# Kernel optimization log

Measured on AMD Instinct MI355X. Metric: run time of the kernel, lower is better.

Reference implementation:

```python
import jax, jax.numpy as jnp
import numpy as np

OBS_LEN = 8
PRED_LEN = 12
BATCH = 65536
EMB = 64
H = 64


def setup_inputs() -> dict:
    key = jax.random.key(0)
    ks = jax.random.split(key, 18)
    s = 1.0 / np.sqrt(H)  # torch default uniform bound scale, used as std here

    def p(k, shape):
        return (jax.random.normal(k, shape, dtype=jnp.float32) * s).astype(jnp.float32)

    return {
        "obs_traj": jax.random.normal(ks[0], (OBS_LEN, BATCH, 2), dtype=jnp.float32),
        "obs_traj_rel": jax.random.normal(ks[1], (OBS_LEN, BATCH, 2), dtype=jnp.float32),
        # encoder params
        "enc_emb_w": p(ks[2], (EMB, 2)),
        "enc_emb_b": p(ks[3], (EMB,)),
        "enc_w_ih": p(ks[4], (4 * H, EMB)),
        "enc_w_hh": p(ks[5], (4 * H, H)),
        "enc_b_ih": p(ks[6], (4 * H,)),
        "enc_b_hh": p(ks[7], (4 * H,)),
        # decoder params
        "dec_emb_w": p(ks[8], (EMB, 2)),
        "dec_emb_b": p(ks[9], (EMB,)),
        "dec_w_ih": p(ks[10], (4 * H, EMB)),
        "dec_w_hh": p(ks[11], (4 * H, H)),
        "dec_b_ih": p(ks[12], (4 * H,)),
        "dec_b_hh": p(ks[13], (4 * H,)),
        "h2p_w": p(ks[14], (2, H)),
        "h2p_b": p(ks[15], (2,)),
    }


def _lstm_cell(h, c, x, w_ih, w_hh, b_ih, b_hh):
    # torch nn.LSTM gate order: i, f, g, o
    gates = x @ w_ih.T + h @ w_hh.T + (b_ih + b_hh)
    i, f, g, o = jnp.split(gates, 4, axis=-1)
    c_new = jax.nn.sigmoid(f) * c + jax.nn.sigmoid(i) * jnp.tanh(g)
    h_new = jax.nn.sigmoid(o) * jnp.tanh(c_new)
    return h_new, c_new


def reference(obs_traj, obs_traj_rel,
              enc_emb_w, enc_emb_b, enc_w_ih, enc_w_hh, enc_b_ih, enc_b_hh,
              dec_emb_w, dec_emb_b, dec_w_ih, dec_w_hh, dec_b_ih, dec_b_hh,
              h2p_w, h2p_b):
    batch = obs_traj_rel.shape[1]

    # ---------- Encoder ----------
    enc_in = obs_traj_rel @ enc_emb_w.T + enc_emb_b  # [T, B, EMB]

    def enc_step(carry, x_t):
        h, c = carry
        h, c = _lstm_cell(h, c, x_t, enc_w_ih, enc_w_hh, enc_b_ih, enc_b_hh)
        return (h, c), None

    h0 = jnp.zeros((batch, H), dtype=obs_traj_rel.dtype)
    c0 = jnp.zeros((batch, H), dtype=obs_traj_rel.dtype)
    (h_enc, _), _ = jax.lax.scan(enc_step, (h0, c0), enc_in)

    # ---------- Decoder ----------
    dec_h = h_enc                                   # final encoder hidden seeds decoder
    dec_c = jnp.zeros((batch, H), dtype=obs_traj_rel.dtype)
    last_pos_rel = obs_traj_rel[-1]
    dec_in = last_pos_rel @ dec_emb_w.T + dec_emb_b  # [B, EMB]

    def dec_step(carry, _):
        h, c, x = carry
        h, c = _lstm_cell(h, c, x, dec_w_ih, dec_w_hh, dec_b_ih, dec_b_hh)
        rel_pos = h @ h2p_w.T + h2p_b               # [B, 2]
        x_next = rel_pos @ dec_emb_w.T + dec_emb_b  # [B, EMB]
        return (h, c, x_next), rel_pos

    (_, _, _), pred_traj_fake_rel = jax.lax.scan(
        dec_step, (dec_h, dec_c, dec_in), None, length=PRED_LEN)
    return pred_traj_fake_rel  # [PRED_LEN, B, 2]
```

## Files before the change

### kernel.cpp

```cpp
#include <hip/hip_runtime.h>

#define OBS_LEN 8
#define PRED_LEN 12
#define TILE_B 128
#define NTHREADS 512

typedef __attribute__((ext_vector_type(8))) short short8;
typedef __attribute__((ext_vector_type(4))) float floatx4;
typedef __attribute__((ext_vector_type(2))) float floatx2;
typedef __attribute__((ext_vector_type(4))) unsigned int u32x4;
typedef __attribute__((ext_vector_type(2))) unsigned int u32x2;
typedef unsigned short u16;
typedef unsigned int u32;

#define L2E 1.442695040888963f

__device__ __forceinline__ u16 f2bf(float f) {
  __bf16 b = (__bf16)f;
  return __builtin_bit_cast(u16, b);
}

#if __has_builtin(__builtin_amdgcn_exp2f)
__device__ __forceinline__ float fexp2_(float x) { return __builtin_amdgcn_exp2f(x); }
#else
__device__ __forceinline__ float fexp2_(float x) { return exp2f(x); }
#endif
__device__ __forceinline__ floatx2 exp2v(floatx2 x) {
  floatx2 r;
  r.x = fexp2_(x.x);
  r.y = fexp2_(x.y);
  return r;
}
#if __has_builtin(__builtin_amdgcn_rcpf)
__device__ __forceinline__ floatx2 rcp2(floatx2 x) {
  floatx2 r;
  r.x = __builtin_amdgcn_rcpf(x.x);
  r.y = __builtin_amdgcn_rcpf(x.y);
  return r;
}
#else
__device__ __forceinline__ floatx2 rcp2(floatx2 x) {
  return floatx2{1.0f / x.x, 1.0f / x.y};
}
#endif

__device__ __forceinline__ floatx4 mfma_bf(short8 a, short8 b, floatx4 c) {
  return __builtin_amdgcn_mfma_f32_16x16x32_bf16(a, b, c, 0, 0, 0);
}

__device__ __forceinline__ short8 frag_lo(u32 a) {
  return __builtin_bit_cast(short8, u32x4{a, 0u, 0u, 0u});
}

__device__ __forceinline__ void fold_rank2(const float* __restrict__ wr,
                                           const float* __restrict__ emb_w,
                                           const float* __restrict__ emb_b,
                                           float& A0, float& A1, float& B0) {
  A0 = A1 = B0 = 0.f;
#pragma unroll
  for (int e4 = 0; e4 < 16; ++e4) {
    const floatx4 w = *(const floatx4*)(wr + e4 * 4);
    const floatx4 m0 = *(const floatx4*)(emb_w + e4 * 8);
    const floatx4 m1 = *(const floatx4*)(emb_w + e4 * 8 + 4);
    const floatx4 bb = *(const floatx4*)(emb_b + e4 * 4);
    A0 += w[0] * m0[0] + w[1] * m0[2] + w[2] * m1[0] + w[3] * m1[2];
    A1 += w[0] * m0[1] + w[1] * m0[3] + w[2] * m1[1] + w[3] * m1[3];
    B0 += w[0] * bb[0] + w[1] * bb[1] + w[2] * bb[2] + w[3] * bb[3];
  }
}

__device__ __forceinline__ void stage_w(const float* __restrict__ W,
                                        u16* __restrict__ wS, int tid) {
  for (int slot = tid; slot < 2048; slot += NTHREADS) {
    const int lane = slot & 63, kf = (slot >> 6) & 1, tile = slot >> 7;
    const int g = lane >> 4, l16 = lane & 15;
    const int gate = (tile >> 2) * 64 + (tile & 3) * 16 + l16;
    const float* src = W + gate * 64 + kf * 32 + g * 8;
    const floatx4 w0 = *(const floatx4*)src;
    const floatx4 w1 = *(const floatx4*)(src + 4);
    short8 a;
#pragma unroll
    for (int j = 0; j < 4; ++j) {
      a[j] = (short)f2bf(w0[j]);
      a[j + 4] = (short)f2bf(w1[j]);
    }
    *(short8*)(wS + slot * 8) = a;
  }
}

__device__ __forceinline__ void stage_weff(const float* __restrict__ Whh,
                                           const float* __restrict__ dA0S,
                                           const float* __restrict__ dA1S,
                                           const float* __restrict__ hw0,
                                           const float* __restrict__ hw1,
                                           u16* __restrict__ wS, int tid) {
  for (int slot = tid; slot < 2048; slot += NTHREADS) {
    const int lane = slot & 63, kf = (slot >> 6) & 1, tile = slot >> 7;
    const int g = lane >> 4, l16 = lane & 15;
    const int gate = (tile >> 2) * 64 + (tile & 3) * 16 + l16;
    const int k0 = kf * 32 + g * 8;
    const float a0 = dA0S[gate], a1 = dA1S[gate];
    const float* src = Whh + gate * 64 + k0;
    const floatx4 w0 = *(const floatx4*)src;
    const floatx4 w1 = *(const floatx4*)(src + 4);
    const floatx4 p00 = *(const floatx4*)(hw0 + k0);
    const floatx4 p01 = *(const floatx4*)(hw0 + k0 + 4);
    const floatx4 p10 = *(const floatx4*)(hw1 + k0);
    const floatx4 p11 = *(const floatx4*)(hw1 + k0 + 4);
    short8 a;
#pragma unroll
    for (int j = 0; j < 4; ++j) {
      a[j] = (short)f2bf(w0[j] + a0 * p00[j] + a1 * p10[j]);
      a[j + 4] = (short)f2bf(w1[j] + a0 * p01[j] + a1 * p11[j]);
    }
    *(short8*)(wS + slot * 8) = a;
  }
}

__device__ __forceinline__ void nonlin_store_ut(const floatx4 (&acc)[4],
                                                floatx4& cc,
                                                u16* __restrict__ wrh,
                                                int l16, int g, int ut) {
  const int sw = l16 & 7;
  u32 hpk[2];
#pragma unroll
  for (int p = 0; p < 2; ++p) {
    const floatx2 iv = {acc[0][2 * p], acc[0][2 * p + 1]};
    const floatx2 fv = {acc[1][2 * p], acc[1][2 * p + 1]};
    const floatx2 gv = {acc[2][2 * p], acc[2][2 * p + 1]};
    const floatx2 ov = {acc[3][2 * p], acc[3][2 * p + 1]};
    const floatx2 ei = exp2v(iv * -L2E);
    const floatx2 ef = exp2v(fv * -L2E);
    const floatx2 eg = exp2v(gv * (2.0f * L2E));
    const floatx2 eo = exp2v(ov * -L2E);
    const floatx2 A = ei + 1.0f;
    const floatx2 F = ef + 1.0f;
    const floatx2 Bg = eg + 1.0f;
    const floatx2 P = A * Bg;
    const floatx2 cold = {cc[2 * p], cc[2 * p + 1]};
    const floatx2 num = cold * P + (eg - 1.0f) * F;
    const floatx2 cn = num * rcp2(F * P);
    cc[2 * p] = cn.x;
    cc[2 * p + 1] = cn.y;
    const floatx2 ec = exp2v(cn * (2.0f * L2E));
    const floatx2 h = (ec - 1.0f) * rcp2((eo + 1.0f) * (ec + 1.0f));
    hpk[p] = (u32)f2bf(h.x) | ((u32)f2bf(h.y) << 16);
  }
  *(u32x2*)(wrh + l16 * 64 + (((ut * 2 + (g >> 1)) ^ sw) * 8) + (g & 1) * 4) =
      u32x2{hpk[0], hpk[1]};
}

template <int PH>
__device__ __forceinline__ void ut_group(int ut, floatx4& cc,
                                         short8 hb0, short8 hb1, short8 pfv,
                                         const u16* __restrict__ wp,
                                         const u32* __restrict__ pafp,
                                         const float* __restrict__ biasp,
                                         u16* __restrict__ wrh,
                                         int g, int l16) {
  floatx4 acc[4];
#pragma unroll
  for (int tg = 0; tg < 4; ++tg) {
    const int tile = tg * 4 + ut;
    const floatx4 biasv = *(const floatx4*)(biasp + tg * 64 + ut * 16 + g * 4);
    if (PH == 0) {
      const u32 pa = (g == 0) ? pafp[tile * 16 + l16] : 0u;
      acc[tg] = mfma_bf(frag_lo(pa), pfv, biasv);
    } else {
      acc[tg] = biasv;
    }
    acc[tg] = mfma_bf(*(const short8*)(wp + (tile * 2 + 1) * 512), hb1, acc[tg]);
    acc[tg] = mfma_bf(*(const short8*)(wp + (tile * 2 + 0) * 512), hb0, acc[tg]);
  }
  nonlin_store_ut(acc, cc, wrh, l16, g, ut);
}

__global__ void __launch_bounds__(NTHREADS, 4)
lstm_kernel(const float* __restrict__ obs_rel,
            const float* __restrict__ enc_emb_w, const float* __restrict__ enc_emb_b,
            const float* __restrict__ enc_w_ih, const float* __restrict__ enc_w_hh,
            const float* __restrict__ enc_b_ih, const float* __restrict__ enc_b_hh,
            const float* __restrict__ dec_emb_w, const float* __restrict__ dec_emb_b,
            const float* __restrict__ dec_w_ih, const float* __restrict__ dec_w_hh,
            const float* __restrict__ dec_b_ih, const float* __restrict__ dec_b_hh,
            const float* __restrict__ h2p_w, const float* __restrict__ h2p_b,
            float* __restrict__ out, int batch) {
  __shared__ __align__(16) u16 wS[16384];
  __shared__ __align__(16) u16 hP[8 * 1024];
  __shared__ __align__(16) float biasS[3][256];
  __shared__ __align__(16) u32 pafS[2][256];
  __shared__ __align__(16) u32 posP[OBS_LEN * TILE_B];
  __shared__ __align__(16) float hw0S[64], hw1S[64];
  __shared__ __align__(16) float dA0S[256], dA1S[256];

  const int tid = threadIdx.x;
  const int wv = tid >> 6, lane = tid & 63;
  const int g = lane >> 4, l16 = lane & 15;
  const long S0 = (long)blockIdx.x * TILE_B;

  for (int i = tid; i < OBS_LEN * TILE_B; i += NTHREADS) {
    const int t = i >> 7, s = i & 127;
    const floatx2 pp = *(const floatx2*)(obs_rel + (long)t * batch * 2 + (S0 + s) * 2);
    posP[i] = (u32)f2bf(pp.x) | ((u32)f2bf(pp.y) << 16);
  }
  if (tid < 64) {
    hw0S[tid] = h2p_w[tid];
    hw1S[tid] = h2p_w[64 + tid];
  }
  const float hb2p0 = h2p_b[0], hb2p1 = h2p_b[1];
  if (tid < 256) {
    const int t = tid >> 6, u6 = tid & 63;
    const int pidx = (t * 4 + (u6 >> 4)) * 16 + (u6 & 15);
    float A0, A1, B0;
    fold_rank2(enc_w_ih + tid * 64, enc_emb_w, enc_emb_b, A0, A1, B0);
    pafS[0][pidx] = (u32)f2bf(A0) | ((u32)f2bf(A1) << 16);
    biasS[0][tid] = enc_b_ih[tid] + enc_b_hh[tid] + B0;
    fold_rank2(dec_w_ih + tid * 64, dec_emb_w, dec_emb_b, A0, A1, B0);
    pafS[1][pidx] = (u32)f2bf(A0) | ((u32)f2bf(A1) << 16);
    dA0S[tid] = A0;
    dA1S[tid] = A1;
    const float db = dec_b_ih[tid] + dec_b_hh[tid] + B0;
    biasS[1][tid] = db;
    biasS[2][tid] = db + A0 * hb2p0 + A1 * hb2p1;
  }
  stage_w(enc_w_hh, wS, tid);
  for (int i = tid; i < 4096; i += NTHREADS) ((u32*)hP)[i] = 0;
  __syncthreads();

  u16* hw = hP + wv * 1024;
  const u16* wp = wS + lane * 8;
  const int sw8 = l16 & 7;
  floatx4 c0{0.f, 0.f, 0.f, 0.f}, c1{0.f, 0.f, 0.f, 0.f};
  floatx4 c2v{0.f, 0.f, 0.f, 0.f}, c3{0.f, 0.f, 0.f, 0.f};

#pragma unroll 1
  for (int t = 0; t < OBS_LEN; ++t) {
    const u16* hr = hw + l16 * 64;
    const short8 hb0 = *(const short8*)(hr + ((g ^ sw8) * 8));
    const short8 hb1 = *(const short8*)(hr + (((4 + g) ^ sw8) * 8));
    const u32 pp = (g == 0) ? posP[t * TILE_B + wv * 16 + l16] : 0u;
    const short8 pfv = frag_lo(pp);
    ut_group<0>(0, c0, hb0, hb1, pfv, wp, &pafS[0][0], &biasS[0][0], hw, g, l16);
    __builtin_amdgcn_sched_barrier(0);
    ut_group<0>(1, c1, hb0, hb1, pfv, wp, &pafS[0][0], &biasS[0][0], hw, g, l16);
    __builtin_amdgcn_sched_barrier(0);
    ut_group<0>(2, c2v, hb0, hb1, pfv, wp, &pafS[0][0], &biasS[0][0], hw, g, l16);
    __builtin_amdgcn_sched_barrier(0);
    ut_group<0>(3, c3, hb0, hb1, pfv, wp, &pafS[0][0], &biasS[0][0], hw, g, l16);
  }

  __syncthreads();
  stage_w(dec_w_hh, wS, tid);
  __syncthreads();
  c0 = c1 = c2v = c3 = floatx4{0.f, 0.f, 0.f, 0.f};
  {
    const u16* hr = hw + l16 * 64;
    const short8 hb0 = *(const short8*)(hr + ((g ^ sw8) * 8));
    const short8 hb1 = *(const short8*)(hr + (((4 + g) ^ sw8) * 8));
    const u32 pp = (g == 0) ? posP[7 * TILE_B + wv * 16 + l16] : 0u;
    const short8 pfv = frag_lo(pp);
    ut_group<0>(0, c0, hb0, hb1, pfv, wp, &pafS[1][0], &biasS[1][0], hw, g, l16);
    __builtin_amdgcn_sched_barrier(0);
    ut_group<0>(1, c1, hb0, hb1, pfv, wp, &pafS[1][0], &biasS[1][0], hw, g, l16);
    __builtin_amdgcn_sched_barrier(0);
    ut_group<0>(2, c2v, hb0, hb1, pfv, wp, &pafS[1][0], &biasS[1][0], hw, g, l16);
    __builtin_amdgcn_sched_barrier(0);
    ut_group<0>(3, c3, hb0, hb1, pfv, wp, &pafS[1][0], &biasS[1][0], hw, g, l16);
  }
  __syncthreads();
  stage_weff(dec_w_hh, dA0S, dA1S, hw0S, hw1S, wS, tid);
  __syncthreads();

  short8 xf0, xf1;
#pragma unroll
  for (int kf = 0; kf < 2; ++kf) {
    const int kb = kf * 32 + g * 8;
    short8 a;
#pragma unroll
    for (int j = 0; j < 8; ++j) {
      const float r = (l16 == 0) ? hw0S[kb + j] : (l16 == 1) ? hw1S[kb + j] : 0.f;
      a[j] = (short)f2bf(r);
    }
    if (kf == 0) xf0 = a; else xf1 = a;
  }

  const floatx4 zero4{0.f, 0.f, 0.f, 0.f};
#pragma unroll 1
  for (int j = 1; j < PRED_LEN; ++j) {
    const u16* hr = hw + l16 * 64;
    const short8 hb0 = *(const short8*)(hr + ((g ^ sw8) * 8));
    const short8 hb1 = *(const short8*)(hr + (((4 + g) ^ sw8) * 8));
    floatx4 ar = mfma_bf(xf0, hb0, zero4);
    ar = mfma_bf(xf1, hb1, ar);
    if (g == 0)
      *(floatx2*)(out + (long)(j - 1) * batch * 2 + (S0 + wv * 16 + l16) * 2) =
          floatx2{ar[0] + hb2p0, ar[1] + hb2p1};
    ut_group<1>(0, c0, hb0, hb1, xf0, wp, &pafS[1][0], &biasS[2][0], hw, g, l16);
    __builtin_amdgcn_sched_barrier(0);
    ut_group<1>(1, c1, hb0, hb1, xf0, wp, &pafS[1][0], &biasS[2][0], hw, g, l16);
    __builtin_amdgcn_sched_barrier(0);
    ut_group<1>(2, c2v, hb0, hb1, xf0, wp, &pafS[1][0], &biasS[2][0], hw, g, l16);
    __builtin_amdgcn_sched_barrier(0);
    ut_group<1>(3, c3, hb0, hb1, xf0, wp, &pafS[1][0], &biasS[2][0], hw, g, l16);
  }

  {
    const u16* hr = hw + l16 * 64;
    const short8 hb0 = *(const short8*)(hr + ((g ^ sw8) * 8));
    const short8 hb1 = *(const short8*)(hr + (((4 + g) ^ sw8) * 8));
    floatx4 ar = mfma_bf(xf0, hb0, zero4);
    ar = mfma_bf(xf1, hb1, ar);
    if (g == 0)
      *(floatx2*)(out + (long)(PRED_LEN - 1) * batch * 2 + (S0 + wv * 16 + l16) * 2) =
          floatx2{ar[0] + hb2p0, ar[1] + hb2p1};
  }
}

extern "C" void kernel_launch(void* const* d_in, const int* in_sizes, int n_in,
                              void* d_out, int out_size, void* d_ws, size_t ws_size,
                              hipStream_t stream) {
  const float* obs_rel = (const float*)d_in[1];
  const int batch = in_sizes[1] / (OBS_LEN * 2);

  const int blocks = batch / TILE_B;
  hipLaunchKernelGGL(lstm_kernel, dim3(blocks), dim3(NTHREADS), 0, stream,
                     obs_rel,
                     (const float*)d_in[2], (const float*)d_in[3],
                     (const float*)d_in[4], (const float*)d_in[5],
                     (const float*)d_in[6], (const float*)d_in[7],
                     (const float*)d_in[8], (const float*)d_in[9],
                     (const float*)d_in[10], (const float*)d_in[11],
                     (const float*)d_in[12], (const float*)d_in[13],
                     (const float*)d_in[14], (const float*)d_in[15],
                     (float*)d_out, batch);
}
```

Measured before the change: 196.4 us.

## Keep recurrent weights in registers and give each wave two batch subtiles

Blocks shrink to 256 threads (4 waves), and each wave now handles 32 batch rows as two 16-row chunks instead of one. The W_hh MFMA fragments are loaded once per phase into a 32-entry short8 register array. They are reused across both chunks and all timesteps, which removes the per-step LDS weight reads. The cost is much higher VGPR pressure, with launch bounds relaxed to 2 blocks per CU, so fewer resident waves remain to hide MFMA, transcendental and LDS latency.

```diff
diff --git a/kernel.cpp b/kernel.cpp
--- a/kernel.cpp
+++ b/kernel.cpp
@@ -3,7 +3,7 @@
 #define OBS_LEN 8
 #define PRED_LEN 12
 #define TILE_B 128
-#define NTHREADS 512
+#define NTHREADS 256
 
 typedef __attribute__((ext_vector_type(8))) short short8;
 typedef __attribute__((ext_vector_type(4))) float floatx4;
@@ -117,11 +117,19 @@
   }
 }
 
+__device__ __forceinline__ void load_wf(const u16* __restrict__ wp,
+                                        short8 (&wf)[16][2]) {
+#pragma unroll
+  for (int tile = 0; tile < 16; ++tile)
+#pragma unroll
+    for (int kf = 0; kf < 2; ++kf)
+      wf[tile][kf] = *(const short8*)(wp + (tile * 2 + kf) * 512);
+}
+
 __device__ __forceinline__ void nonlin_store_ut(const floatx4 (&acc)[4],
                                                 floatx4& cc,
-                                                u16* __restrict__ wrh,
-                                                int l16, int g, int ut) {
-  const int sw = l16 & 7;
+                                                u16* __restrict__ wrow,
+                                                int g, int ut, int sw) {
   u32 hpk[2];
 #pragma unroll
   for (int p = 0; p < 2; ++p) {
@@ -146,36 +154,58 @@
     const floatx2 h = (ec - 1.0f) * rcp2((eo + 1.0f) * (ec + 1.0f));
     hpk[p] = (u32)f2bf(h.x) | ((u32)f2bf(h.y) << 16);
   }
-  *(u32x2*)(wrh + l16 * 64 + (((ut * 2 + (g >> 1)) ^ sw) * 8) + (g & 1) * 4) =
+  *(u32x2*)(wrow + (((ut * 2 + (g >> 1)) ^ sw) * 8) + (g & 1) * 4) =
       u32x2{hpk[0], hpk[1]};
 }
 
-template <int PH>
-__device__ __forceinline__ void ut_group(int ut, floatx4& cc,
-                                         short8 hb0, short8 hb1, short8 pfv,
-                                         const u16* __restrict__ wp,
-                                         const u32* __restrict__ pafp,
-                                         const float* __restrict__ biasp,
-                                         u16* __restrict__ wrh,
-                                         int g, int l16) {
-  floatx4 acc[4];
-#pragma unroll
-  for (int tg = 0; tg < 4; ++tg) {
-    const int tile = tg * 4 + ut;
-    const floatx4 biasv = *(const floatx4*)(biasp + tg * 64 + ut * 16 + g * 4);
+template <int PH, int REL>
+__device__ __forceinline__ void step_all(
+    const short8 (&wf)[16][2], floatx4 (&c)[8], u16* __restrict__ hw,
+    const u32* __restrict__ pafp, const float* __restrict__ biasp,
+    const u32* __restrict__ posrow, short8 xf0, short8 xf1,
+    float hb2p0, float hb2p1, float* __restrict__ outp, long sbase,
+    int wv, int g, int l16, int sw8) {
+#pragma unroll
+  for (int n = 0; n < 2; ++n) {
+    u16* wrow = hw + (n * 16 + l16) * 64;
+    const short8 hb0 = *(const short8*)(wrow + ((g ^ sw8) * 8));
+    const short8 hb1 = *(const short8*)(wrow + (((4 + g) ^ sw8) * 8));
+    short8 pfv = short8{0, 0, 0, 0, 0, 0, 0, 0};
     if (PH == 0) {
-      const u32 pa = (g == 0) ? pafp[tile * 16 + l16] : 0u;
-      acc[tg] = mfma_bf(frag_lo(pa), pfv, biasv);
-    } else {
-      acc[tg] = biasv;
-    }
-    acc[tg] = mfma_bf(*(const short8*)(wp + (tile * 2 + 1) * 512), hb1, acc[tg]);
-    acc[tg] = mfma_bf(*(const short8*)(wp + (tile * 2 + 0) * 512), hb0, acc[tg]);
-  }
-  nonlin_store_ut(acc, cc, wrh, l16, g, ut);
-}
-
-__global__ void __launch_bounds__(NTHREADS, 4)
+      const u32 pp = (g == 0) ? posrow[wv * 32 + n * 16 + l16] : 0u;
+      pfv = frag_lo(pp);
+    }
+    if (REL) {
+      floatx4 ar = mfma_bf(xf0, hb0, floatx4{0.f, 0.f, 0.f, 0.f});
+      ar = mfma_bf(xf1, hb1, ar);
+      if (g == 0)
+        *(floatx2*)(outp + (sbase + n * 16 + l16) * 2) =
+            floatx2{ar[0] + hb2p0, ar[1] + hb2p1};
+    }
+#pragma unroll
+    for (int ut = 0; ut < 4; ++ut) {
+      floatx4 acc[4];
+#pragma unroll
+      for (int tg = 0; tg < 4; ++tg) {
+        const int tile = tg * 4 + ut;
+        const floatx4 biasv =
+            *(const floatx4*)(biasp + tg * 64 + ut * 16 + g * 4);
+        if (PH == 0) {
+          const u32 pa = (g == 0) ? pafp[tile * 16 + l16] : 0u;
+          acc[tg] = mfma_bf(frag_lo(pa), pfv, biasv);
+        } else {
+          acc[tg] = biasv;
+        }
+        acc[tg] = mfma_bf(wf[tile][1], hb1, acc[tg]);
+        acc[tg] = mfma_bf(wf[tile][0], hb0, acc[tg]);
+      }
+      nonlin_store_ut(acc, c[n * 4 + ut], wrow, g, ut, sw8);
+      __builtin_amdgcn_sched_barrier(0);
+    }
+  }
+}
+
+__global__ void __launch_bounds__(NTHREADS, 2)
 lstm_kernel(const float* __restrict__ obs_rel,
             const float* __restrict__ enc_emb_w, const float* __restrict__ enc_emb_b,
             const float* __restrict__ enc_w_ih, const float* __restrict__ enc_w_hh,
@@ -186,7 +216,7 @@
             const float* __restrict__ h2p_w, const float* __restrict__ h2p_b,
             float* __restrict__ out, int batch) {
   __shared__ __align__(16) u16 wS[16384];
-  __shared__ __align__(16) u16 hP[8 * 1024];
+  __shared__ __align__(16) u16 hP[4 * 2048];
   __shared__ __align__(16) float biasS[3][256];
   __shared__ __align__(16) u32 pafS[2][256];
   __shared__ __align__(16) u32 posP[OBS_LEN * TILE_B];
@@ -208,7 +238,7 @@
     hw1S[tid] = h2p_w[64 + tid];
   }
   const float hb2p0 = h2p_b[0], hb2p1 = h2p_b[1];
-  if (tid < 256) {
+  {
     const int t = tid >> 6, u6 = tid & 63;
     const int pidx = (t * 4 + (u6 >> 4)) * 16 + (u6 & 15);
     float A0, A1, B0;
@@ -227,49 +257,36 @@
   for (int i = tid; i < 4096; i += NTHREADS) ((u32*)hP)[i] = 0;
   __syncthreads();
 
-  u16* hw = hP + wv * 1024;
+  u16* hw = hP + wv * 2048;
   const u16* wp = wS + lane * 8;
   const int sw8 = l16 & 7;
-  floatx4 c0{0.f, 0.f, 0.f, 0.f}, c1{0.f, 0.f, 0.f, 0.f};
-  floatx4 c2v{0.f, 0.f, 0.f, 0.f}, c3{0.f, 0.f, 0.f, 0.f};
+  const long sbase = S0 + wv * 32;
+
+  short8 wf[16][2];
+  load_wf(wp, wf);
+  floatx4 c[8];
+#pragma unroll
+  for (int i = 0; i < 8; ++i) c[i] = floatx4{0.f, 0.f, 0.f, 0.f};
+  const short8 z8 = short8{0, 0, 0, 0, 0, 0, 0, 0};
 
 #pragma unroll 1
   for (int t = 0; t < OBS_LEN; ++t) {
-    const u16* hr = hw + l16 * 64;
-    const short8 hb0 = *(const short8*)(hr + ((g ^ sw8) * 8));
-    const short8 hb1 = *(const short8*)(hr + (((4 + g) ^ sw8) * 8));
-    const u32 pp = (g == 0) ? posP[t * TILE_B + wv * 16 + l16] : 0u;
-    const short8 pfv = frag_lo(pp);
-    ut_group<0>(0, c0, hb0, hb1, pfv, wp, &pafS[0][0], &biasS[0][0], hw, g, l16);
-    __builtin_amdgcn_sched_barrier(0);
-    ut_group<0>(1, c1, hb0, hb1, pfv, wp, &pafS[0][0], &biasS[0][0], hw, g, l16);
-    __builtin_amdgcn_sched_barrier(0);
-    ut_group<0>(2, c2v, hb0, hb1, pfv, wp, &pafS[0][0], &biasS[0][0], hw, g, l16);
-    __builtin_amdgcn_sched_barrier(0);
-    ut_group<0>(3, c3, hb0, hb1, pfv, wp, &pafS[0][0], &biasS[0][0], hw, g, l16);
+    step_all<0, 0>(wf, c, hw, &pafS[0][0], &biasS[0][0], posP + t * TILE_B,
+                   z8, z8, 0.f, 0.f, out, sbase, wv, g, l16, sw8);
   }
 
   __syncthreads();
   stage_w(dec_w_hh, wS, tid);
   __syncthreads();
-  c0 = c1 = c2v = c3 = floatx4{0.f, 0.f, 0.f, 0.f};
-  {
-    const u16* hr = hw + l16 * 64;
-    const short8 hb0 = *(const short8*)(hr + ((g ^ sw8) * 8));
-    const short8 hb1 = *(const short8*)(hr + (((4 + g) ^ sw8) * 8));
-    const u32 pp = (g == 0) ? posP[7 * TILE_B + wv * 16 + l16] : 0u;
-    const short8 pfv = frag_lo(pp);
-    ut_group<0>(0, c0, hb0, hb1, pfv, wp, &pafS[1][0], &biasS[1][0], hw, g, l16);
-    __builtin_amdgcn_sched_barrier(0);
-    ut_group<0>(1, c1, hb0, hb1, pfv, wp, &pafS[1][0], &biasS[1][0], hw, g, l16);
-    __builtin_amdgcn_sched_barrier(0);
-    ut_group<0>(2, c2v, hb0, hb1, pfv, wp, &pafS[1][0], &biasS[1][0], hw, g, l16);
-    __builtin_amdgcn_sched_barrier(0);
-    ut_group<0>(3, c3, hb0, hb1, pfv, wp, &pafS[1][0], &biasS[1][0], hw, g, l16);
-  }
+  load_wf(wp, wf);
+#pragma unroll
+  for (int i = 0; i < 8; ++i) c[i] = floatx4{0.f, 0.f, 0.f, 0.f};
+  step_all<0, 0>(wf, c, hw, &pafS[1][0], &biasS[1][0], posP + 7 * TILE_B,
+                 z8, z8, 0.f, 0.f, out, sbase, wv, g, l16, sw8);
   __syncthreads();
   stage_weff(dec_w_hh, dA0S, dA1S, hw0S, hw1S, wS, tid);
   __syncthreads();
+  load_wf(wp, wf);
 
   short8 xf0, xf1;
 #pragma unroll
@@ -284,34 +301,23 @@
     if (kf == 0) xf0 = a; else xf1 = a;
   }
 
-  const floatx4 zero4{0.f, 0.f, 0.f, 0.f};
 #pragma unroll 1
   for (int j = 1; j < PRED_LEN; ++j) {
-    const u16* hr = hw + l16 * 64;
+    step_all<1, 1>(wf, c, hw, &pafS[1][0], &biasS[2][0], posP,
+                   xf0, xf1, hb2p0, hb2p1,
+                   out + (long)(j - 1) * batch * 2, sbase, wv, g, l16, sw8);
+  }
+
+#pragma unroll
+  for (int n = 0; n < 2; ++n) {
+    const u16* hr = hw + (n * 16 + l16) * 64;
     const short8 hb0 = *(const short8*)(hr + ((g ^ sw8) * 8));
     const short8 hb1 = *(const short8*)(hr + (((4 + g) ^ sw8) * 8));
-    floatx4 ar = mfma_bf(xf0, hb0, zero4);
+    floatx4 ar = mfma_bf(xf0, hb0, floatx4{0.f, 0.f, 0.f, 0.f});
     ar = mfma_bf(xf1, hb1, ar);
     if (g == 0)
-      *(floatx2*)(out + (long)(j - 1) * batch * 2 + (S0 + wv * 16 + l16) * 2) =
-          floatx2{ar[0] + hb2p0, ar[1] + hb2p1};
-    ut_group<1>(0, c0, hb0, hb1, xf0, wp, &pafS[1][0], &biasS[2][0], hw, g, l16);
-    __builtin_amdgcn_sched_barrier(0);
-    ut_group<1>(1, c1, hb0, hb1, xf0, wp, &pafS[1][0], &biasS[2][0], hw, g, l16);
-    __builtin_amdgcn_sched_barrier(0);
-    ut_group<1>(2, c2v, hb0, hb1, xf0, wp, &pafS[1][0], &biasS[2][0], hw, g, l16);
-    __builtin_amdgcn_sched_barrier(0);
-    ut_group<1>(3, c3, hb0, hb1, xf0, wp, &pafS[1][0], &biasS[2][0], hw, g, l16);
-  }
-
-  {
-    const u16* hr = hw + l16 * 64;
-    const short8 hb0 = *(const short8*)(hr + ((g ^ sw8) * 8));
-    const short8 hb1 = *(const short8*)(hr + (((4 + g) ^ sw8) * 8));
-    floatx4 ar = mfma_bf(xf0, hb0, zero4);
-    ar = mfma_bf(xf1, hb1, ar);
-    if (g == 0)
-      *(floatx2*)(out + (long)(PRED_LEN - 1) * batch * 2 + (S0 + wv * 16 + l16) * 2) =
+      *(floatx2*)(out + (long)(PRED_LEN - 1) * batch * 2 +
+                  (sbase + n * 16 + l16) * 2) =
           floatx2{ar[0] + hb2p0, ar[1] + hb2p1};
   }
 }
```

Result: slower. 209.4 us (+6.7%).
